# Performance work log

Measured on AMD Instinct MI355X. Metric: run time of the kernel, lower is better.

## Reference

```python
import jax, jax.numpy as jnp
import numpy as np

K = 32
START = K - 2  # index of <START>
STOP = K - 1   # index of <STOP>
NEG = -10000.0
B, T = 512, 2048


def setup_inputs() -> dict:
    key = jax.random.key(0)
    k1, k2, k3, k4 = jax.random.split(key, 4)
    feats = jax.random.normal(k1, (B, T, K), dtype=jnp.float32)
    transitions = jax.random.normal(k2, (K, K), dtype=jnp.float32)
    # constraints set in __init__: never transition TO START, never FROM STOP
    transitions = transitions.at[START, :].set(NEG).at[:, STOP].set(NEG)
    tags = jax.random.randint(k3, (B, T), 0, K - 2)          # real tags only
    lens = jnp.maximum(jax.random.randint(k4, (B,), 0, T), 1)  # at least 1 token
    return {"feats": feats, "transitions": transitions, "tags": tags, "lens": lens}


def _crf_loss(feats, transitions, tags, lens):
    Bn, Tn, Kn = feats.shape
    # ---- forward algorithm (log-partition) ----
    init = jnp.full((Bn, Kn), NEG, feats.dtype).at[:, START].set(0.0)

    def step(alpha, emit):
        # alpha[b,prev] + trans[next,prev] -> logsumexp over prev, then + emit[b,next]
        nxt = jax.scipy.special.logsumexp(
            alpha[:, None, :] + transitions[None, :, :], axis=2) + emit
        return nxt, nxt

    _, alphas = jax.lax.scan(step, init, jnp.swapaxes(feats, 0, 1))  # [T,B,K]
    alphas = jnp.concatenate([init[None], alphas], axis=0)           # [T+1,B,K]
    alpha_at_len = alphas[lens, jnp.arange(Bn)]                      # [B,K]
    forward_score = jax.scipy.special.logsumexp(
        alpha_at_len + transitions[STOP][None, :], axis=1)           # [B]

    # ---- gold score ----
    tags_stop = jnp.where(jnp.arange(Tn)[None, :] < lens[:, None], tags, STOP)
    pad_start = jnp.concatenate(
        [jnp.full((Bn, 1), START, tags.dtype), tags], axis=1)        # [B,T+1]
    pad_stop = jnp.concatenate(
        [tags_stop, jnp.full((Bn, 1), STOP, tags.dtype)], axis=1)    # [B,T+1]
    trans_mask = jnp.arange(Tn + 1)[None, :] <= lens[:, None]        # len+1 transitions
    trans_sc = jnp.where(trans_mask, transitions[pad_stop, pad_start], 0.0).sum(axis=1)
    emit_mask = jnp.arange(Tn)[None, :] < lens[:, None]
    emit_sc = jnp.where(
        emit_mask,
        jnp.take_along_axis(feats, tags[:, :, None], axis=2)[..., 0],
        0.0).sum(axis=1)
    gold_score = trans_sc + emit_sc

    return jnp.mean(forward_score - gold_score)


def reference(feats, transitions, tags, lens):
    return _crf_loss(feats, transitions, tags, lens)
```

## Files before the change

### kernel.cpp

```cpp
#include <hip/hip_runtime.h>
#include <hip/hip_bf16.h>
#include <cstdint>
#include <cstddef>

#define Kn 32
#define Bn 512
#define Tn 2048
#define CH 128
#define NC (Tn / CH)
#define GP 8
#define MMB (Bn * NC / 4)
#define GB (Bn * GP / 4)
#define START 30
#define STOP 31
#define LN2F 0.69314718055994530942f

typedef __attribute__((ext_vector_type(8))) short bf16x8;
typedef __attribute__((ext_vector_type(16))) float f32x16;

union BF8 { bf16x8 v; unsigned u[4]; };

__device__ __forceinline__ unsigned pk2(float lo, float hi) {
  return __builtin_amdgcn_perm(__float_as_uint(hi) + 0x8000u,
                               __float_as_uint(lo) + 0x8000u, 0x07060302u);
}

__device__ __forceinline__ float bcast32(float v, int idx) {
  return __shfl(v, idx, 32);
}

__global__ __launch_bounds__(256, 6) void crf_fused(
    const float* __restrict__ feats, const float* __restrict__ trans,
    const int* __restrict__ tags, const int* __restrict__ lens,
    float* __restrict__ pmats, float* __restrict__ poffs,
    float* __restrict__ gold_part) {
  const int wid = threadIdx.x >> 6;
  const int lane = threadIdx.x & 63;

  if (blockIdx.x < MMB) {
    const int idx = blockIdx.x * 4 + wid;
    const int c = idx >> 9;
    const int b = idx & (Bn - 1);
    const int len = lens[b];
    const int nsteps = min(max(len - c * CH, 0), CH);
    if (nsteps == 0) return;

    const int m = lane & 31;
    const int h = lane >> 5;

    float e1[8], e2[8];
    {
      const float* tr = trans + m * Kn + 8 * h;
#pragma unroll
      for (int j = 0; j < 8; ++j) {
        e1[j] = __expf(tr[j]) * 0.0078125f;
        e2[j] = __expf(tr[16 + j]) * 0.0078125f;
      }
    }

    unsigned b1u[4] = {0, 0, 0, 0}, b2u[4] = {0, 0, 0, 0};
    {
      int j = m - 8 * h;
      if (0 <= j && j < 8) b1u[j >> 1] |= (j & 1) ? 0x3F800000u : 0x00003F80u;
      j = m - 16 - 8 * h;
      if (0 <= j && j < 8) b2u[j >> 1] |= (j & 1) ? 0x3F800000u : 0x00003F80u;
    }

    const f32x16 zf = {0.f, 0.f, 0.f, 0.f, 0.f, 0.f, 0.f, 0.f,
                       0.f, 0.f, 0.f, 0.f, 0.f, 0.f, 0.f, 0.f};
    f32x16 acc;
    float off = 0.0f;

    const int t0 = c * CH;
    const float* fb = feats + ((size_t)b * Tn + t0) * Kn + m;
    const int lim = Tn - 1 - t0;

    float ring[8];
#pragma unroll
    for (int i = 0; i < 8; ++i) ring[i] = fb[(size_t)min(i, lim) * Kn];

    auto mmstep = [&](float f, bool rn) {
      const float w = __expf(f);
      BF8 A1, A2, B1, B2;
#pragma unroll
      for (int j = 0; j < 4; ++j) {
        A1.u[j] = pk2(e1[2 * j] * w, e1[2 * j + 1] * w);
        A2.u[j] = pk2(e2[2 * j] * w, e2[2 * j + 1] * w);
        B1.u[j] = b1u[j];
        B2.u[j] = b2u[j];
      }
      acc = __builtin_amdgcn_mfma_f32_32x32x16_bf16(A2.v, B2.v, zf, 0, 0, 0);
      acc = __builtin_amdgcn_mfma_f32_32x32x16_bf16(A1.v, B1.v, acc, 0, 0, 0);

      if (rn) {
        float mx = acc[0];
#pragma unroll
        for (int r = 1; r < 16; ++r) mx = fmaxf(mx, acc[r]);
#pragma unroll
        for (int d = 1; d < 64; d <<= 1) mx = fmaxf(mx, __shfl_xor(mx, d));
        const int e = (int)((__float_as_uint(mx) >> 23) & 255u);
        const float sc = __uint_as_float((unsigned)(254 - e) << 23);
#pragma unroll
        for (int r = 0; r < 16; ++r) acc[r] *= sc;
        off += (float)(e - 127) * LN2F;
      }

      unsigned q[8];
#pragma unroll
      for (int i = 0; i < 8; ++i) q[i] = pk2(acc[2 * i], acc[2 * i + 1]);
      const unsigned r1 = __shfl_xor(h ? q[0] : q[2], 32);
      const unsigned r2 = __shfl_xor(h ? q[1] : q[3], 32);
      const unsigned r3 = __shfl_xor(h ? q[4] : q[6], 32);
      const unsigned r4 = __shfl_xor(h ? q[5] : q[7], 32);
      b1u[0] = h ? r1 : q[0];
      b1u[1] = h ? r2 : q[1];
      b1u[2] = h ? q[2] : r1;
      b1u[3] = h ? q[3] : r2;
      b2u[0] = h ? r3 : q[4];
      b2u[1] = h ? r4 : q[5];
      b2u[2] = h ? q[6] : r3;
      b2u[3] = h ? q[7] : r4;
    };

    int t = 0;
    const int nb = nsteps >> 3;
    for (int mb = 0; mb < nb; ++mb) {
#pragma unroll
      for (int i = 0; i < 8; ++i) {
        const float f = ring[i];
        ring[i] = fb[(size_t)min(t + i + 8, lim) * Kn];
        mmstep(f, ((t + i) & 31) == 31);
      }
      t += 8;
    }
    const int rem = nsteps & 7;
    for (int i = 0; i < rem; ++i) mmstep(ring[i], false);

    float* pm = pmats + (size_t)(b * NC + c) * (Kn * Kn);
#pragma unroll
    for (int r = 0; r < 16; ++r) {
      const int row = (r & 3) + 8 * (r >> 2) + 4 * h;
      pm[row * Kn + m] = acc[r];
    }
    if (lane == 0) poffs[b * NC + c] = off + 7.0f * LN2F * (float)nsteps;
  } else {
    const int g = (blockIdx.x - MMB) * 4 + wid;
    const int b = g >> 3, p = g & 7;
    const int len = lens[b];
    const int t0 = p * 256;
    const int t1 = min(t0 + 256, len);
    const int* tg = tags + (size_t)b * Tn;
    const float* fbp = feats + (size_t)b * Tn * Kn;
    float acc = 0.f;
    for (int tt = t0 + lane; tt < t1; tt += 64) {
      const int tag = tg[tt];
      const int prev = tt ? tg[tt - 1] : START;
      acc += fbp[(size_t)tt * Kn + tag] + trans[tag * Kn + prev];
    }
    if (lane == 0 && ((len - 1) >> 8) == p)
      acc += trans[STOP * Kn + tg[len - 1]];
#pragma unroll
    for (int msk = 32; msk >= 1; msk >>= 1) acc += __shfl_xor(acc, msk);
    if (lane == 0) gold_part[b * GP + p] = acc;
  }
}

__device__ __forceinline__ float renorm_s(float& s, float off) {
  int e = (int)((__float_as_uint(s) >> 23) & 255u);
  e = max(e, __shfl_xor(e, 1));
  e = max(e, __shfl_xor(e, 2));
  e = max(e, __shfl_xor(e, 4));
  e = max(e, __shfl_xor(e, 8));
  e = max(e, __shfl_xor(e, 16));
  s *= __uint_as_float((unsigned)(254 - e) << 23);
  return off + (float)(e - 127) * LN2F;
}

__global__ __launch_bounds__(64, 1) void crf_apply(
    const float* __restrict__ trans, const int* __restrict__ lens,
    const float* __restrict__ pmats, const float* __restrict__ poffs,
    float* __restrict__ fscore) {
  const int lane = threadIdx.x;
  const int b = blockIdx.x;
  const int n = lane & 31;
  const int hb = (lane >> 5) * 16;
  const int len = lens[b];
  const int nc = (len + CH - 1) / CH;
  float s = (n == START) ? 1.0f : 0.0f;
  float off = 0.0f;
  for (int c = 0; c < nc; ++c) {
    const float* pm = pmats + (size_t)(b * NC + c) * (Kn * Kn) + n * Kn + hb;
    const float4 p0 = *(const float4*)pm;
    const float4 p1 = *(const float4*)(pm + 4);
    const float4 p2 = *(const float4*)(pm + 8);
    const float4 p3 = *(const float4*)(pm + 12);
    float a0 = 0.f, a1 = 0.f, a2 = 0.f, a3 = 0.f;
    a0 = fmaf(bcast32(s, hb + 0), p0.x, a0);
    a0 = fmaf(bcast32(s, hb + 1), p0.y, a0);
    a0 = fmaf(bcast32(s, hb + 2), p0.z, a0);
    a0 = fmaf(bcast32(s, hb + 3), p0.w, a0);
    a1 = fmaf(bcast32(s, hb + 4), p1.x, a1);
    a1 = fmaf(bcast32(s, hb + 5), p1.y, a1);
    a1 = fmaf(bcast32(s, hb + 6), p1.z, a1);
    a1 = fmaf(bcast32(s, hb + 7), p1.w, a1);
    a2 = fmaf(bcast32(s, hb + 8), p2.x, a2);
    a2 = fmaf(bcast32(s, hb + 9), p2.y, a2);
    a2 = fmaf(bcast32(s, hb + 10), p2.z, a2);
    a2 = fmaf(bcast32(s, hb + 11), p2.w, a2);
    a3 = fmaf(bcast32(s, hb + 12), p3.x, a3);
    a3 = fmaf(bcast32(s, hb + 13), p3.y, a3);
    a3 = fmaf(bcast32(s, hb + 14), p3.z, a3);
    a3 = fmaf(bcast32(s, hb + 15), p3.w, a3);
    float p = (a0 + a1) + (a2 + a3);
    p += __shfl_xor(p, 32);
    s = p;
    off = renorm_s(s, off);
    off += poffs[b * NC + c];
  }
  const float es = __expf(trans[STOP * Kn + n]);
  float q = s * es;
#pragma unroll
  for (int d = 1; d < 32; d <<= 1) q += __shfl_xor(q, d);
  if (lane == 0) fscore[b] = __logf(q) + off;
}

__device__ __forceinline__ float crf_step_slow(float s, float eemit,
                                               const float (&er)[16], int hb) {
  float a0 = 0.f, a1 = 0.f, a2 = 0.f, a3 = 0.f;
#pragma unroll
  for (int j = 0; j < 4; ++j) {
    a0 = fmaf(bcast32(s, hb + j), er[j], a0);
    a1 = fmaf(bcast32(s, hb + 4 + j), er[4 + j], a1);
    a2 = fmaf(bcast32(s, hb + 8 + j), er[8 + j], a2);
    a3 = fmaf(bcast32(s, hb + 12 + j), er[12 + j], a3);
  }
  float p = (a0 + a1) + (a2 + a3);
  p += __shfl_xor(p, 32);
  return p * eemit;
}

__global__ __launch_bounds__(64, 1) void crf_main(
    const float* __restrict__ feats, const float* __restrict__ trans,
    const int* __restrict__ tags, const int* __restrict__ lens,
    float* __restrict__ fscore, float* __restrict__ gold_part) {
  const int lane = threadIdx.x;
  if (blockIdx.x < Bn) {
    const int b = blockIdx.x;
    const int n = lane & 31;
    const int hb = (lane >> 5) * 16;
    float er[16], estop[16];
#pragma unroll
    for (int j = 0; j < 16; ++j) {
      er[j] = __expf(trans[n * Kn + hb + j]);
      estop[j] = __expf(trans[STOP * Kn + hb + j]);
    }
    const int len = lens[b];
    const float* fbase = feats + ((size_t)b * Tn) * Kn + n;
    float s = (n == START) ? 1.0f : 0.0f;
    float off = 0.0f;
    float fbuf[8];
#pragma unroll
    for (int i = 0; i < 8; ++i) fbuf[i] = fbase[(size_t)i * Kn];
    int t = 0;
    const int nm = len >> 3;
    for (int m2 = 0; m2 < nm; ++m2) {
#pragma unroll
      for (int i = 0; i < 8; ++i) {
        const float f = fbuf[i];
        const int tp = t + i + 8;
        if (tp < Tn) fbuf[i] = fbase[(size_t)tp * Kn];
        s = crf_step_slow(s, __expf(f), er, hb);
        if ((i & 3) == 3) off = renorm_s(s, off);
      }
      t += 8;
    }
    const int rem = len & 7;
    for (int i = 0; i < rem; ++i) {
      const float f = fbase[(size_t)(t + i) * Kn];
      s = crf_step_slow(s, __expf(f), er, hb);
      off = renorm_s(s, off);
    }
    float a0 = 0.f, a1 = 0.f, a2 = 0.f, a3 = 0.f;
#pragma unroll
    for (int j = 0; j < 4; ++j) {
      a0 = fmaf(bcast32(s, hb + j), estop[j], a0);
      a1 = fmaf(bcast32(s, hb + 4 + j), estop[4 + j], a1);
      a2 = fmaf(bcast32(s, hb + 8 + j), estop[8 + j], a2);
      a3 = fmaf(bcast32(s, hb + 12 + j), estop[12 + j], a3);
    }
    float p = (a0 + a1) + (a2 + a3);
    p += __shfl_xor(p, 32);
    if (lane == 0) fscore[b] = __logf(p) + off;
  } else {
    const int b = blockIdx.x - Bn;
    const int len = lens[b];
    const int* tg = tags + (size_t)b * Tn;
    const float* fb = feats + (size_t)b * Tn * Kn;
    float acc = 0.f;
    for (int tt = lane; tt < len; tt += 64) {
      const int tag = tg[tt];
      const int prev = (tt == 0) ? START : tg[tt - 1];
      acc += fb[(size_t)tt * Kn + tag] + trans[tag * Kn + prev];
    }
    if (lane == 0) acc += trans[STOP * Kn + tg[len - 1]];
#pragma unroll
    for (int msk = 32; msk >= 1; msk >>= 1) acc += __shfl_xor(acc, msk);
    if (lane == 0) gold_part[b * GP] = acc;
    else if (lane < GP) gold_part[b * GP + lane] = 0.f;
  }
}

__global__ __launch_bounds__(64, 1) void crf_reduce(
    const float* __restrict__ fscore, const float* __restrict__ gold_part,
    float* __restrict__ out) {
  const int lane = threadIdx.x;
  float acc = 0.f;
  for (int i = lane; i < Bn; i += 64) {
    float gp = 0.f;
#pragma unroll
    for (int p = 0; p < GP; ++p) gp += gold_part[i * GP + p];
    acc += fscore[i] - gp;
  }
#pragma unroll
  for (int msk = 32; msk >= 1; msk >>= 1) acc += __shfl_xor(acc, msk);
  if (lane == 0) out[0] = acc * (1.0f / (float)Bn);
}

extern "C" void kernel_launch(void* const* d_in, const int* in_sizes, int n_in,
                              void* d_out, int out_size, void* d_ws, size_t ws_size,
                              hipStream_t stream) {
  const float* feats = (const float*)d_in[0];
  const float* trans = (const float*)d_in[1];
  const int* tags = (const int*)d_in[2];
  const int* lens = (const int*)d_in[3];

  float* fscore = (float*)d_ws;
  float* gold_part = fscore + Bn;
  float* poffs = gold_part + (size_t)Bn * GP;
  float* pmats = poffs + (size_t)Bn * NC;
  const size_t need =
      ((size_t)Bn + (size_t)Bn * GP + (size_t)Bn * NC +
       (size_t)Bn * NC * Kn * Kn) * sizeof(float);
  if (ws_size >= need) {
    crf_fused<<<MMB + GB, 256, 0, stream>>>(feats, trans, tags, lens, pmats,
                                            poffs, gold_part);
    crf_apply<<<Bn, 64, 0, stream>>>(trans, lens, pmats, poffs, fscore);
  } else {
    crf_main<<<2 * Bn, 64, 0, stream>>>(feats, trans, tags, lens, fscore,
                                        gold_part);
  }
  crf_reduce<<<1, 64, 0, stream>>>(fscore, gold_part, (float*)d_out);
}
```

Baseline: 290.4 us.

## Use persistent atomic work queue, truncating bf16 pack, and fold reduction into apply

Turns the fused chunk-matrix kernel into a persistent kernel: a fixed grid of blocks whose waves pull work items from a global atomic counter. Waves assigned empty chunks no longer occupy launched blocks, and setup such as exp(trans) is computed once per wave. The bf16 pack switches from round-to-nearest to truncation, and the shuffle exchange is restructured to eight unconditional xor-shuffles. The separate reduce kernel and the fallback path are removed: crf_apply atomically accumulates into the output after a memset. The float atomic sum makes the result order-nondeterministic, and truncation slightly lowers precision.

```diff
diff --git a/kernel.cpp b/kernel.cpp
--- a/kernel.cpp
+++ b/kernel.cpp
@@ -9,8 +9,9 @@
 #define CH 128
 #define NC (Tn / CH)
 #define GP 8
-#define MMB (Bn * NC / 4)
-#define GB (Bn * GP / 4)
+#define NITEMS (Bn * NC)
+#define GITEMS (Bn * GP)
+#define PBLK 2048
 #define START 30
 #define STOP 31
 #define LN2F 0.69314718055994530942f
@@ -20,148 +21,163 @@
 
 union BF8 { bf16x8 v; unsigned u[4]; };
 
-__device__ __forceinline__ unsigned pk2(float lo, float hi) {
-  return __builtin_amdgcn_perm(__float_as_uint(hi) + 0x8000u,
-                               __float_as_uint(lo) + 0x8000u, 0x07060302u);
+__device__ __forceinline__ unsigned pk2z(float lo, float hi) {
+  return __builtin_amdgcn_perm(__float_as_uint(hi), __float_as_uint(lo),
+                               0x07060302u);
 }
 
 __device__ __forceinline__ float bcast32(float v, int idx) {
   return __shfl(v, idx, 32);
 }
 
-__global__ __launch_bounds__(256, 6) void crf_fused(
+__global__ __launch_bounds__(256, 8) void crf_fused(
     const float* __restrict__ feats, const float* __restrict__ trans,
     const int* __restrict__ tags, const int* __restrict__ lens,
     float* __restrict__ pmats, float* __restrict__ poffs,
-    float* __restrict__ gold_part) {
-  const int wid = threadIdx.x >> 6;
+    float* __restrict__ gold_part, int* __restrict__ ctr) {
   const int lane = threadIdx.x & 63;
-
-  if (blockIdx.x < MMB) {
-    const int idx = blockIdx.x * 4 + wid;
-    const int c = idx >> 9;
-    const int b = idx & (Bn - 1);
-    const int len = lens[b];
-    const int nsteps = min(max(len - c * CH, 0), CH);
-    if (nsteps == 0) return;
-
-    const int m = lane & 31;
-    const int h = lane >> 5;
-
-    float e1[8], e2[8];
-    {
-      const float* tr = trans + m * Kn + 8 * h;
-#pragma unroll
-      for (int j = 0; j < 8; ++j) {
-        e1[j] = __expf(tr[j]) * 0.0078125f;
-        e2[j] = __expf(tr[16 + j]) * 0.0078125f;
+  const int m = lane & 31;
+  const int h = lane >> 5;
+
+  float e1[8], e2[8];
+  {
+    const float* tr = trans + m * Kn + 8 * h;
+#pragma unroll
+    for (int j = 0; j < 8; ++j) {
+      e1[j] = __expf(tr[j]) * 0.0078125f;
+      e2[j] = __expf(tr[16 + j]) * 0.0078125f;
+    }
+  }
+  unsigned i1[4] = {0, 0, 0, 0}, i2[4] = {0, 0, 0, 0};
+  {
+    int j = m - 8 * h;
+    if (0 <= j && j < 8) i1[j >> 1] = (j & 1) ? 0x3F800000u : 0x00003F80u;
+    j = m - 16 - 8 * h;
+    if (0 <= j && j < 8) i2[j >> 1] = (j & 1) ? 0x3F800000u : 0x00003F80u;
+  }
+  const f32x16 zf = {0.f, 0.f, 0.f, 0.f, 0.f, 0.f, 0.f, 0.f,
+                     0.f, 0.f, 0.f, 0.f, 0.f, 0.f, 0.f, 0.f};
+
+  for (;;) {
+    int item;
+    if (lane == 0) item = atomicAdd(ctr, 1);
+    item = __shfl(item, 0);
+    if (item >= NITEMS + GITEMS) break;
+
+    if (item < NITEMS) {
+      const int c = item >> 9;
+      const int b = item & (Bn - 1);
+      const int len = lens[b];
+      const int nsteps = min(max(len - c * CH, 0), CH);
+      if (nsteps == 0) continue;
+
+      unsigned b1u[4], b2u[4];
+#pragma unroll
+      for (int j = 0; j < 4; ++j) { b1u[j] = i1[j]; b2u[j] = i2[j]; }
+
+      f32x16 acc;
+      float off = 0.0f;
+      const int t0 = c * CH;
+      const float* fb = feats + ((size_t)b * Tn + t0) * Kn + m;
+      const int lim = Tn - 1 - t0;
+
+      float ring[8];
+#pragma unroll
+      for (int i = 0; i < 8; ++i) ring[i] = fb[(size_t)min(i, lim) * Kn];
+
+      auto mmstep = [&](float f, bool rn) {
+        const float w = __expf(f);
+        BF8 A1, A2, B1, B2;
+#pragma unroll
+        for (int j = 0; j < 4; ++j) {
+          A1.u[j] = pk2z(e1[2 * j] * w, e1[2 * j + 1] * w);
+          A2.u[j] = pk2z(e2[2 * j] * w, e2[2 * j + 1] * w);
+          B1.u[j] = b1u[j];
+          B2.u[j] = b2u[j];
+        }
+        acc = __builtin_amdgcn_mfma_f32_32x32x16_bf16(A2.v, B2.v, zf, 0, 0, 0);
+        acc = __builtin_amdgcn_mfma_f32_32x32x16_bf16(A1.v, B1.v, acc, 0, 0, 0);
+
+        if (rn) {
+          float mx = acc[0];
+#pragma unroll
+          for (int r = 1; r < 16; ++r) mx = fmaxf(mx, acc[r]);
+#pragma unroll
+          for (int d = 1; d < 64; d <<= 1) mx = fmaxf(mx, __shfl_xor(mx, d));
+          const int e = (int)((__float_as_uint(mx) >> 23) & 255u);
+          const float sc = __uint_as_float((unsigned)(254 - e) << 23);
+#pragma unroll
+          for (int r = 0; r < 16; ++r) acc[r] *= sc;
+          off += (float)(e - 127) * LN2F;
+        }
+
+        const unsigned qa = pk2z(acc[0], acc[1]);
+        const unsigned qb = pk2z(acc[2], acc[3]);
+        const unsigned qc = pk2z(acc[4], acc[5]);
+        const unsigned qd = pk2z(acc[6], acc[7]);
+        const unsigned qe = pk2z(acc[8], acc[9]);
+        const unsigned qf = pk2z(acc[10], acc[11]);
+        const unsigned qg = pk2z(acc[12], acc[13]);
+        const unsigned qh = pk2z(acc[14], acc[15]);
+        const unsigned ra = __shfl_xor(qa, 32);
+        const unsigned rb = __shfl_xor(qb, 32);
+        const unsigned rc = __shfl_xor(qc, 32);
+        const unsigned rd = __shfl_xor(qd, 32);
+        const unsigned re = __shfl_xor(qe, 32);
+        const unsigned rf = __shfl_xor(qf, 32);
+        const unsigned rg = __shfl_xor(qg, 32);
+        const unsigned rh = __shfl_xor(qh, 32);
+        b1u[0] = h ? rc : qa;
+        b1u[1] = h ? rd : qb;
+        b1u[2] = h ? qc : ra;
+        b1u[3] = h ? qd : rb;
+        b2u[0] = h ? rg : qe;
+        b2u[1] = h ? rh : qf;
+        b2u[2] = h ? qg : re;
+        b2u[3] = h ? qh : rf;
+      };
+
+      int t = 0;
+      const int nb = nsteps >> 3;
+      for (int mb = 0; mb < nb; ++mb) {
+#pragma unroll
+        for (int i = 0; i < 8; ++i) {
+          const float f = ring[i];
+          ring[i] = fb[(size_t)min(t + i + 8, lim) * Kn];
+          mmstep(f, ((t + i) & 31) == 31);
+        }
+        t += 8;
       }
+      const int rem = nsteps & 7;
+      for (int i = 0; i < rem; ++i) mmstep(ring[i], false);
+
+      float* pm = pmats + (size_t)(b * NC + c) * (Kn * Kn);
+#pragma unroll
+      for (int r = 0; r < 16; ++r) {
+        const int row = (r & 3) + 8 * (r >> 2) + 4 * h;
+        pm[row * Kn + m] = acc[r];
+      }
+      if (lane == 0) poffs[b * NC + c] = off + 7.0f * LN2F * (float)nsteps;
+    } else {
+      const int g = item - NITEMS;
+      const int b = g >> 3, p = g & 7;
+      const int len = lens[b];
+      const int t0 = p * 256;
+      const int t1 = min(t0 + 256, len);
+      const int* tg = tags + (size_t)b * Tn;
+      const float* fbp = feats + (size_t)b * Tn * Kn;
+      float acc = 0.f;
+      for (int tt = t0 + lane; tt < t1; tt += 64) {
+        const int tag = tg[tt];
+        const int prev = tt ? tg[tt - 1] : START;
+        acc += fbp[(size_t)tt * Kn + tag] + trans[tag * Kn + prev];
+      }
+      if (lane == 0 && ((len - 1) >> 8) == p)
+        acc += trans[STOP * Kn + tg[len - 1]];
+#pragma unroll
+      for (int msk = 32; msk >= 1; msk >>= 1) acc += __shfl_xor(acc, msk);
+      if (lane == 0) gold_part[b * GP + p] = acc;
     }
-
-    unsigned b1u[4] = {0, 0, 0, 0}, b2u[4] = {0, 0, 0, 0};
-    {
-      int j = m - 8 * h;
-      if (0 <= j && j < 8) b1u[j >> 1] |= (j & 1) ? 0x3F800000u : 0x00003F80u;
-      j = m - 16 - 8 * h;
-      if (0 <= j && j < 8) b2u[j >> 1] |= (j & 1) ? 0x3F800000u : 0x00003F80u;
-    }
-
-    const f32x16 zf = {0.f, 0.f, 0.f, 0.f, 0.f, 0.f, 0.f, 0.f,
-                       0.f, 0.f, 0.f, 0.f, 0.f, 0.f, 0.f, 0.f};
-    f32x16 acc;
-    float off = 0.0f;
-
-    const int t0 = c * CH;
-    const float* fb = feats + ((size_t)b * Tn + t0) * Kn + m;
-    const int lim = Tn - 1 - t0;
-
-    float ring[8];
-#pragma unroll
-    for (int i = 0; i < 8; ++i) ring[i] = fb[(size_t)min(i, lim) * Kn];
-
-    auto mmstep = [&](float f, bool rn) {
-      const float w = __expf(f);
-      BF8 A1, A2, B1, B2;
-#pragma unroll
-      for (int j = 0; j < 4; ++j) {
-        A1.u[j] = pk2(e1[2 * j] * w, e1[2 * j + 1] * w);
-        A2.u[j] = pk2(e2[2 * j] * w, e2[2 * j + 1] * w);
-        B1.u[j] = b1u[j];
-        B2.u[j] = b2u[j];
-      }
-      acc = __builtin_amdgcn_mfma_f32_32x32x16_bf16(A2.v, B2.v, zf, 0, 0, 0);
-      acc = __builtin_amdgcn_mfma_f32_32x32x16_bf16(A1.v, B1.v, acc, 0, 0, 0);
-
-      if (rn) {
-        float mx = acc[0];
-#pragma unroll
-        for (int r = 1; r < 16; ++r) mx = fmaxf(mx, acc[r]);
-#pragma unroll
-        for (int d = 1; d < 64; d <<= 1) mx = fmaxf(mx, __shfl_xor(mx, d));
-        const int e = (int)((__float_as_uint(mx) >> 23) & 255u);
-        const float sc = __uint_as_float((unsigned)(254 - e) << 23);
-#pragma unroll
-        for (int r = 0; r < 16; ++r) acc[r] *= sc;
-        off += (float)(e - 127) * LN2F;
-      }
-
-      unsigned q[8];
-#pragma unroll
-      for (int i = 0; i < 8; ++i) q[i] = pk2(acc[2 * i], acc[2 * i + 1]);
-      const unsigned r1 = __shfl_xor(h ? q[0] : q[2], 32);
-      const unsigned r2 = __shfl_xor(h ? q[1] : q[3], 32);
-      const unsigned r3 = __shfl_xor(h ? q[4] : q[6], 32);
-      const unsigned r4 = __shfl_xor(h ? q[5] : q[7], 32);
-      b1u[0] = h ? r1 : q[0];
-      b1u[1] = h ? r2 : q[1];
-      b1u[2] = h ? q[2] : r1;
-      b1u[3] = h ? q[3] : r2;
-      b2u[0] = h ? r3 : q[4];
-      b2u[1] = h ? r4 : q[5];
-      b2u[2] = h ? q[6] : r3;
-      b2u[3] = h ? q[7] : r4;
-    };
-
-    int t = 0;
-    const int nb = nsteps >> 3;
-    for (int mb = 0; mb < nb; ++mb) {
-#pragma unroll
-      for (int i = 0; i < 8; ++i) {
-        const float f = ring[i];
-        ring[i] = fb[(size_t)min(t + i + 8, lim) * Kn];
-        mmstep(f, ((t + i) & 31) == 31);
-      }
-      t += 8;
-    }
-    const int rem = nsteps & 7;
-    for (int i = 0; i < rem; ++i) mmstep(ring[i], false);
-
-    float* pm = pmats + (size_t)(b * NC + c) * (Kn * Kn);
-#pragma unroll
-    for (int r = 0; r < 16; ++r) {
-      const int row = (r & 3) + 8 * (r >> 2) + 4 * h;
-      pm[row * Kn + m] = acc[r];
-    }
-    if (lane == 0) poffs[b * NC + c] = off + 7.0f * LN2F * (float)nsteps;
-  } else {
-    const int g = (blockIdx.x - MMB) * 4 + wid;
-    const int b = g >> 3, p = g & 7;
-    const int len = lens[b];
-    const int t0 = p * 256;
-    const int t1 = min(t0 + 256, len);
-    const int* tg = tags + (size_t)b * Tn;
-    const float* fbp = feats + (size_t)b * Tn * Kn;
-    float acc = 0.f;
-    for (int tt = t0 + lane; tt < t1; tt += 64) {
-      const int tag = tg[tt];
-      const int prev = tt ? tg[tt - 1] : START;
-      acc += fbp[(size_t)tt * Kn + tag] + trans[tag * Kn + prev];
-    }
-    if (lane == 0 && ((len - 1) >> 8) == p)
-      acc += trans[STOP * Kn + tg[len - 1]];
-#pragma unroll
-    for (int msk = 32; msk >= 1; msk >>= 1) acc += __shfl_xor(acc, msk);
-    if (lane == 0) gold_part[b * GP + p] = acc;
   }
 }
 
@@ -179,7 +195,7 @@
 __global__ __launch_bounds__(64, 1) void crf_apply(
     const float* __restrict__ trans, const int* __restrict__ lens,
     const float* __restrict__ pmats, const float* __restrict__ poffs,
-    float* __restrict__ fscore) {
+    const float* __restrict__ gold_part, float* __restrict__ out) {
   const int lane = threadIdx.x;
   const int b = blockIdx.x;
   const int n = lane & 31;
@@ -221,109 +237,13 @@
   float q = s * es;
 #pragma unroll
   for (int d = 1; d < 32; d <<= 1) q += __shfl_xor(q, d);
-  if (lane == 0) fscore[b] = __logf(q) + off;
-}
-
-__device__ __forceinline__ float crf_step_slow(float s, float eemit,
-                                               const float (&er)[16], int hb) {
-  float a0 = 0.f, a1 = 0.f, a2 = 0.f, a3 = 0.f;
-#pragma unroll
-  for (int j = 0; j < 4; ++j) {
-    a0 = fmaf(bcast32(s, hb + j), er[j], a0);
-    a1 = fmaf(bcast32(s, hb + 4 + j), er[4 + j], a1);
-    a2 = fmaf(bcast32(s, hb + 8 + j), er[8 + j], a2);
-    a3 = fmaf(bcast32(s, hb + 12 + j), er[12 + j], a3);
-  }
-  float p = (a0 + a1) + (a2 + a3);
-  p += __shfl_xor(p, 32);
-  return p * eemit;
-}
-
-__global__ __launch_bounds__(64, 1) void crf_main(
-    const float* __restrict__ feats, const float* __restrict__ trans,
-    const int* __restrict__ tags, const int* __restrict__ lens,
-    float* __restrict__ fscore, float* __restrict__ gold_part) {
-  const int lane = threadIdx.x;
-  if (blockIdx.x < Bn) {
-    const int b = blockIdx.x;
-    const int n = lane & 31;
-    const int hb = (lane >> 5) * 16;
-    float er[16], estop[16];
-#pragma unroll
-    for (int j = 0; j < 16; ++j) {
-      er[j] = __expf(trans[n * Kn + hb + j]);
-      estop[j] = __expf(trans[STOP * Kn + hb + j]);
-    }
-    const int len = lens[b];
-    const float* fbase = feats + ((size_t)b * Tn) * Kn + n;
-    float s = (n == START) ? 1.0f : 0.0f;
-    float off = 0.0f;
-    float fbuf[8];
-#pragma unroll
-    for (int i = 0; i < 8; ++i) fbuf[i] = fbase[(size_t)i * Kn];
-    int t = 0;
-    const int nm = len >> 3;
-    for (int m2 = 0; m2 < nm; ++m2) {
-#pragma unroll
-      for (int i = 0; i < 8; ++i) {
-        const float f = fbuf[i];
-        const int tp = t + i + 8;
-        if (tp < Tn) fbuf[i] = fbase[(size_t)tp * Kn];
-        s = crf_step_slow(s, __expf(f), er, hb);
-        if ((i & 3) == 3) off = renorm_s(s, off);
-      }
-      t += 8;
-    }
-    const int rem = len & 7;
-    for (int i = 0; i < rem; ++i) {
-      const float f = fbase[(size_t)(t + i) * Kn];
-      s = crf_step_slow(s, __expf(f), er, hb);
-      off = renorm_s(s, off);
-    }
-    float a0 = 0.f, a1 = 0.f, a2 = 0.f, a3 = 0.f;
-#pragma unroll
-    for (int j = 0; j < 4; ++j) {
-      a0 = fmaf(bcast32(s, hb + j), estop[j], a0);
-      a1 = fmaf(bcast32(s, hb + 4 + j), estop[4 + j], a1);
-      a2 = fmaf(bcast32(s, hb + 8 + j), estop[8 + j], a2);
-      a3 = fmaf(bcast32(s, hb + 12 + j), estop[12 + j], a3);
-    }
-    float p = (a0 + a1) + (a2 + a3);
-    p += __shfl_xor(p, 32);
-    if (lane == 0) fscore[b] = __logf(p) + off;
-  } else {
-    const int b = blockIdx.x - Bn;
-    const int len = lens[b];
-    const int* tg = tags + (size_t)b * Tn;
-    const float* fb = feats + (size_t)b * Tn * Kn;
-    float acc = 0.f;
-    for (int tt = lane; tt < len; tt += 64) {
-      const int tag = tg[tt];
-      const int prev = (tt == 0) ? START : tg[tt - 1];
-      acc += fb[(size_t)tt * Kn + tag] + trans[tag * Kn + prev];
-    }
-    if (lane == 0) acc += trans[STOP * Kn + tg[len - 1]];
-#pragma unroll
-    for (int msk = 32; msk >= 1; msk >>= 1) acc += __shfl_xor(acc, msk);
-    if (lane == 0) gold_part[b * GP] = acc;
-    else if (lane < GP) gold_part[b * GP + lane] = 0.f;
-  }
-}
-
-__global__ __launch_bounds__(64, 1) void crf_reduce(
-    const float* __restrict__ fscore, const float* __restrict__ gold_part,
-    float* __restrict__ out) {
-  const int lane = threadIdx.x;
-  float acc = 0.f;
-  for (int i = lane; i < Bn; i += 64) {
-    float gp = 0.f;
-#pragma unroll
-    for (int p = 0; p < GP; ++p) gp += gold_part[i * GP + p];
-    acc += fscore[i] - gp;
-  }
-#pragma unroll
-  for (int msk = 32; msk >= 1; msk >>= 1) acc += __shfl_xor(acc, msk);
-  if (lane == 0) out[0] = acc * (1.0f / (float)Bn);
+  if (lane == 0) {
+    const float fs = __logf(q) + off;
+    float gs = 0.f;
+#pragma unroll
+    for (int p = 0; p < GP; ++p) gs += gold_part[b * GP + p];
+    atomicAdd(out, (fs - gs) * (1.0f / (float)Bn));
+  }
 }
 
 extern "C" void kernel_launch(void* const* d_in, const int* in_sizes, int n_in,
@@ -334,20 +254,15 @@
   const int* tags = (const int*)d_in[2];
   const int* lens = (const int*)d_in[3];
 
-  float* fscore = (float*)d_ws;
-  float* gold_part = fscore + Bn;
+  int* ctr = (int*)d_ws;
+  float* gold_part = (float*)d_ws + 4;
   float* poffs = gold_part + (size_t)Bn * GP;
   float* pmats = poffs + (size_t)Bn * NC;
-  const size_t need =
-      ((size_t)Bn + (size_t)Bn * GP + (size_t)Bn * NC +
-       (size_t)Bn * NC * Kn * Kn) * sizeof(float);
-  if (ws_size >= need) {
-    crf_fused<<<MMB + GB, 256, 0, stream>>>(feats, trans, tags, lens, pmats,
-                                            poffs, gold_part);
-    crf_apply<<<Bn, 64, 0, stream>>>(trans, lens, pmats, poffs, fscore);
-  } else {
-    crf_main<<<2 * Bn, 64, 0, stream>>>(feats, trans, tags, lens, fscore,
-                                        gold_part);
-  }
-  crf_reduce<<<1, 64, 0, stream>>>(fscore, gold_part, (float*)d_out);
-}
+
+  hipMemsetAsync(ctr, 0, 16, stream);
+  hipMemsetAsync(d_out, 0, (size_t)out_size * sizeof(float), stream);
+  crf_fused<<<PBLK, 256, 0, stream>>>(feats, trans, tags, lens, pmats, poffs,
+                                      gold_part, ctr);
+  crf_apply<<<Bn, 64, 0, stream>>>(trans, lens, pmats, poffs, gold_part,
+                                   (float*)d_out);
+}
```

New measurement: 416.8 us. 1.44x slower.
